# Kernel optimization log

Measured on AMD Instinct MI355X. Metric: run time of the kernel, lower is better.

## Reference

```python
import jax, jax.numpy as jnp
import numpy as np

KSIZE = 7
STRIDE = 4
SCALE = 10.0


def _same_pad(n, k, s):
    # torch 'same' padding used in extract_image_patches (asymmetric)
    out = -(-n // s)
    pad = max(0, (out - 1) * s + k - n)
    top = pad // 2
    return (top, pad - top)


def _conv1x1(x, W, b):
    # x: [C,H,W], W: [O,C], b: [O]
    return jnp.einsum('oc,chw->ohw', W, x) + b[:, None, None]


def _unfold(x, k, s, pad_h, pad_w):
    # x: [C,H,W] -> patches [Lh*Lw, C*k*k] in (C, kh, kw) order (torch Unfold order)
    C = x.shape[0]
    xp = jnp.pad(x, ((0, 0), pad_h, pad_w))
    Hp, Wp = xp.shape[1], xp.shape[2]
    Lh = (Hp - k) // s + 1
    Lw = (Wp - k) // s + 1
    ih = (jnp.arange(Lh) * s)[:, None] + jnp.arange(k)  # [Lh,k]
    iw = (jnp.arange(Lw) * s)[:, None] + jnp.arange(k)  # [Lw,k]
    p = xp[:, ih][:, :, :, iw]                # [C,Lh,k,Lw,k]
    p = p.transpose(1, 3, 0, 2, 4).reshape(Lh * Lw, C * k * k)
    return p, Lh, Lw


def _fold(p, Lh, Lw, C, k, s, H, W, pad):
    # p: [Lh*Lw, C*k*k] -> overlap-summed image [C,H,W] (torch F.fold, symmetric pad)
    P = p.reshape(Lh, Lw, C, k, k).transpose(2, 0, 1, 3, 4)  # [C,Lh,Lw,k,k]
    Hp, Wp = H + 2 * pad, W + 2 * pad
    ih = (jnp.arange(Lh) * s)[:, None] + jnp.arange(k)  # [Lh,k]
    iw = (jnp.arange(Lw) * s)[:, None] + jnp.arange(k)  # [Lw,k]
    IH = ih[:, None, :, None]  # broadcast -> [Lh,Lw,k,k]
    IW = iw[None, :, None, :]
    canvas = jnp.zeros((C, Hp, Wp), p.dtype).at[:, IH, IW].add(P)
    return canvas[:, pad:pad + H, pad:pad + W]


def _salsa_one(x, Wg, bg, Wt, bt, Wp, bp, Ww, bw):
    # x: [C,H,W]
    C, H, W = x.shape
    ic = Wg.shape[0]
    k, s = KSIZE, STRIDE
    ph = _same_pad(H, k, s)
    pw = _same_pad(W, k, s)
    q, Lh, Lw = _unfold(_conv1x1(x, Wg, bg), k, s, ph, pw)   # g   -> queries [L, ic*k*k]
    kk, _, _ = _unfold(_conv1x1(x, Wp, bp), k, s, ph, pw)    # phi -> keys
    v, _, _ = _unfold(_conv1x1(x, Wt, bt), k, s, ph, pw)     # theta -> values
    att = jax.nn.softmax((q @ kk.T) * SCALE, axis=1)         # [L1,L2]
    out = att @ v                                            # [L1, ic*k*k]
    fp = (k - 1) // 2  # paddings[0] from stride-1 same_padding in the original (=3)
    zi = _fold(out, Lh, Lw, ic, k, s, H, W, fp)
    ones_p, mLh, mLw = _unfold(jnp.ones((ic, H, W), x.dtype), k, s, (fp, fp), (fp, fp))
    mask = _fold(ones_p, mLh, mLw, ic, k, s, H, W, fp)
    zi = zi / mask
    return x + _conv1x1(zi, Ww, bw)


def setup_inputs() -> dict:
    key = jax.random.key(0)
    B, C, H, W, IC = 4, 64, 256, 256, 16
    ks = jax.random.split(key, 9)
    sC = 1.0 / np.sqrt(C)
    sI = 1.0 / np.sqrt(IC)
    return {
        'b': jax.random.normal(ks[0], (B, C, H, W), jnp.float32),
        'Wg': jax.random.normal(ks[1], (IC, C), jnp.float32) * sC,
        'bg': jax.random.normal(ks[2], (IC,), jnp.float32) * 0.01,
        'Wt': jax.random.normal(ks[3], (IC, C), jnp.float32) * sC,
        'bt': jax.random.normal(ks[4], (IC,), jnp.float32) * 0.01,
        'Wp': jax.random.normal(ks[5], (IC, C), jnp.float32) * sC,
        'bp': jax.random.normal(ks[6], (IC,), jnp.float32) * 0.01,
        'Ww': jax.random.normal(ks[7], (C, IC), jnp.float32) * sI,
        'bw': jax.random.normal(ks[8], (C,), jnp.float32) * 0.01,
    }


def reference(b, Wg, bg, Wt, bt, Wp, bp, Ww, bw):
    f = jax.vmap(_salsa_one, in_axes=(0, None, None, None, None, None, None, None, None))
    return f(b, Wg, bg, Wt, bt, Wp, bp, Ww, bw)
```

## Files before the change

### kernel.cpp

```cpp
#include <hip/hip_runtime.h>

#define CIN 64
#define ICN 16
#define HH 256
#define WID 256
#define HW (HH*WID)
#define LL 4096
#define KD 784
#define KDP 800
#define KQ 832
#define NVT 896
#define NB 4
#define SPLITK 4
#define KCH (LL/SPLITK)

typedef __attribute__((ext_vector_type(8))) short short8;
typedef __attribute__((ext_vector_type(4))) float f32x4;
typedef __attribute__((ext_vector_type(4))) int i32x4;

__device__ __forceinline__ unsigned short f2bf(float x){
  union { float f; unsigned u; } v; v.f = x;
  unsigned r = v.u + 0x7FFF + ((v.u >> 16) & 1);
  return (unsigned short)(r >> 16);
}

__global__ __launch_bounds__(256) void conv1x1_3(
    const float* __restrict__ x,
    const float* __restrict__ Wg, const float* __restrict__ bg,
    const float* __restrict__ Wp, const float* __restrict__ bp,
    const float* __restrict__ Wt, const float* __restrict__ bt,
    float* __restrict__ G, float* __restrict__ P, float* __restrict__ T) {
  __shared__ float wg[ICN*CIN], wp[ICN*CIN], wt[ICN*CIN];
  int t = threadIdx.x;
  for (int i = t; i < ICN*CIN; i += 256) { wg[i]=Wg[i]; wp[i]=Wp[i]; wt[i]=Wt[i]; }
  __syncthreads();
  int p = blockIdx.x*256 + t;
  float aG[ICN], aP[ICN], aT[ICN];
#pragma unroll
  for (int o=0;o<ICN;o++){ aG[o]=bg[o]; aP[o]=bp[o]; aT[o]=bt[o]; }
  for (int c=0;c<CIN;c++){
    float xv = x[c*HW + p];
#pragma unroll
    for (int o=0;o<ICN;o++){
      aG[o] = fmaf(wg[o*CIN+c], xv, aG[o]);
      aP[o] = fmaf(wp[o*CIN+c], xv, aP[o]);
      aT[o] = fmaf(wt[o*CIN+c], xv, aT[o]);
    }
  }
#pragma unroll
  for (int o=0;o<ICN;o++){ G[o*HW+p]=aG[o]; P[o*HW+p]=aP[o]; T[o*HW+p]=aT[o]; }
}

__global__ __launch_bounds__(256) void unfold_qk_q(
    const float* __restrict__ G, const float* __restrict__ P,
    char* __restrict__ Q0, char* __restrict__ Q1,
    char* __restrict__ K0, char* __restrict__ K1,
    float* __restrict__ sQ, float* __restrict__ sK){
  __shared__ float gb[KQ], pb[KQ];
  __shared__ float redg[256], redp[256];
  int row = blockIdx.x;
  int iy = row >> 6, ix = row & 63;
  int t = threadIdx.x;
  float gmax = 0.f, pmax = 0.f;
  for (int col = t; col < KQ; col += 256){
    float g = 0.f, p = 0.f;
    if (col < KD){
      int c = col / 49; int r = col - c*49; int dy = r / 7; int dx = r - dy*7;
      int y = (iy<<2) + dy - 1, x = (ix<<2) + dx - 1;
      if ((unsigned)y < HH && (unsigned)x < WID){
        int a = c*HW + (y<<8) + x;
        g = G[a]; p = P[a];
      }
    }
    gb[col] = g; pb[col] = p;
    gmax = fmaxf(gmax, fabsf(g)); pmax = fmaxf(pmax, fabsf(p));
  }
  redg[t]=gmax; redp[t]=pmax; __syncthreads();
  for (int s2=128;s2>0;s2>>=1){
    if (t<s2){ redg[t]=fmaxf(redg[t],redg[t+s2]); redp[t]=fmaxf(redp[t],redp[t+s2]); }
    __syncthreads();
  }
  float mg = redg[0], mp = redp[0];
  float rsg = mg > 0.f ? mg*(1.f/127.f) : 1.f;
  float rsp = mp > 0.f ? mp*(1.f/127.f) : 1.f;
  if (t==0){ sQ[row]=rsg; sK[row]=rsp; }
  float ig = 1.f/rsg, ip = 1.f/rsp;
  if (t < KQ/4){
    char q0[4],q1[4],k0[4],k1[4];
#pragma unroll
    for (int u=0;u<4;u++){
      float xg = gb[t*4+u]*ig;
      float a0 = rintf(xg);
      int ia1 = (int)rintf((xg - a0)*256.f);
      ia1 = ia1>127?127:(ia1<-127?-127:ia1);
      q0[u] = (char)(int)a0; q1[u] = (char)ia1;
      float xp = pb[t*4+u]*ip;
      float b0 = rintf(xp);
      int ib1 = (int)rintf((xp - b0)*256.f);
      ib1 = ib1>127?127:(ib1<-127?-127:ib1);
      k0[u] = (char)(int)b0; k1[u] = (char)ib1;
    }
    size_t o = (size_t)row*KQ + t*4;
    *(char4*)(Q0+o) = make_char4(q0[0],q0[1],q0[2],q0[3]);
    *(char4*)(Q1+o) = make_char4(q1[0],q1[1],q1[2],q1[3]);
    *(char4*)(K0+o) = make_char4(k0[0],k0[1],k0[2],k0[3]);
    *(char4*)(K1+o) = make_char4(k1[0],k1[1],k1[2],k1[3]);
  }
}

__global__ __launch_bounds__(256) void unfold_vt(
    const float* __restrict__ T, unsigned short* __restrict__ Vt){
  int idx = blockIdx.x*256 + threadIdx.x;
  int col = idx >> 12, row = idx & 4095;
  float t = 0.f;
  if (col < KD){
    int c = col / 49; int r = col - c*49; int dy = r / 7; int dx = r - dy*7;
    int iy = row >> 6, ix = row & 63;
    int y = (iy<<2) + dy - 1, x = (ix<<2) + dx - 1;
    if ((unsigned)y < HH && (unsigned)x < WID) t = T[c*HW + (y<<8) + x];
  }
  Vt[idx] = f2bf(t);
}

__global__ __launch_bounds__(256) void gemm_qk_i8(
    const char* __restrict__ Q0, const char* __restrict__ Q1,
    const char* __restrict__ K0, const char* __restrict__ K1,
    const float* __restrict__ sQ, const float* __restrict__ sK,
    float* __restrict__ ATT){
  __shared__ alignas(16) char lds[4][128*64];
  const int tid = threadIdx.x;
  const int lane = tid & 63, w = tid >> 6;
  const int wr = w >> 1, wc = w & 1;
  const int row0 = blockIdx.y*128, col0 = blockIdx.x*128;

  const char* base;
  { const char* s0[4] = {
      Q0 + (size_t)row0*KQ, Q1 + (size_t)row0*KQ,
      K0 + (size_t)col0*KQ, K1 + (size_t)col0*KQ };
    base = s0[w]; }

  const int r_lo = lane >> 2, slot = lane & 3;
  int goff[8];
#pragma unroll
  for (int j=0;j<8;j++){
    int r = j*16 + r_lo;
    goff[j] = r*KQ + ((slot ^ ((r>>1)&3))<<4);
  }

  const int lrow = lane & 15, g = lane >> 4;
  int offA[4], offB[4];
#pragma unroll
  for (int i=0;i<4;i++){
    int rA = wr*64 + i*16 + lrow;
    offA[i] = rA*64 + ((g ^ ((rA>>1)&3))<<4);
    int rB = wc*64 + i*16 + lrow;
    offB[i] = rB*64 + ((g ^ ((rB>>1)&3))<<4);
  }

  i32x4 accH[4][4] = {};
  i32x4 accC[4][4] = {};

  for (int kb = 0; kb < KQ; kb += 64){
#pragma unroll
    for (int j=0;j<8;j++)
      __builtin_amdgcn_global_load_lds(
        (const __attribute__((address_space(1))) void*)(base + goff[j] + kb),
        (__attribute__((address_space(3))) void*)(&lds[w][j*1024]), 16, 0, 0);
    __syncthreads();
    i32x4 a0[4], a1[4], b0[4], b1[4];
#pragma unroll
    for (int i=0;i<4;i++){
      a0[i] = *(const i32x4*)&lds[0][offA[i]];
      a1[i] = *(const i32x4*)&lds[1][offA[i]];
      b0[i] = *(const i32x4*)&lds[2][offB[i]];
      b1[i] = *(const i32x4*)&lds[3][offB[i]];
    }
#pragma unroll
    for (int i=0;i<4;i++)
#pragma unroll
      for (int j=0;j<4;j++){
        accH[i][j] = __builtin_amdgcn_mfma_i32_16x16x64_i8(a0[i], b0[j], accH[i][j], 0,0,0);
        accC[i][j] = __builtin_amdgcn_mfma_i32_16x16x64_i8(a0[i], b1[j], accC[i][j], 0,0,0);
        accC[i][j] = __builtin_amdgcn_mfma_i32_16x16x64_i8(a1[i], b0[j], accC[i][j], 0,0,0);
      }
    __syncthreads();
  }

#pragma unroll
  for (int j=0;j<4;j++){
    int col = col0 + wc*64 + j*16 + lrow;
    float cs = sK[col]*10.f;
#pragma unroll
    for (int i=0;i<4;i++){
#pragma unroll
      for (int r=0;r<4;r++){
        int row = row0 + wr*64 + i*16 + g*4 + r;
        float rs = sQ[row];
        ATT[(size_t)row*LL + col] =
          rs*cs*((float)accH[i][j][r] + (float)accC[i][j][r]*0.00390625f);
      }
    }
  }
}

__global__ __launch_bounds__(256) void softmax_rows(
    const float* __restrict__ ATT, unsigned short* __restrict__ Pb){
  __shared__ float red[256];
  int t = threadIdx.x;
  const float4* r4 = (const float4*)(ATT + (size_t)blockIdx.x * LL);
  ushort4* po = (ushort4*)(Pb + (size_t)blockIdx.x * LL);
  float4 v[4];
  float mx = -3.4e38f;
#pragma unroll
  for (int i=0;i<4;i++){
    v[i] = r4[t + (i<<8)];
    mx = fmaxf(mx, fmaxf(fmaxf(v[i].x, v[i].y), fmaxf(v[i].z, v[i].w)));
  }
  red[t] = mx; __syncthreads();
  for (int s2=128;s2>0;s2>>=1){ if (t<s2) red[t]=fmaxf(red[t],red[t+s2]); __syncthreads(); }
  mx = red[0]; __syncthreads();
  float sum = 0.f;
#pragma unroll
  for (int i=0;i<4;i++){
    v[i].x = __expf(v[i].x-mx); v[i].y = __expf(v[i].y-mx);
    v[i].z = __expf(v[i].z-mx); v[i].w = __expf(v[i].w-mx);
    sum += v[i].x + v[i].y + v[i].z + v[i].w;
  }
  red[t]=sum; __syncthreads();
  for (int s2=128;s2>0;s2>>=1){ if (t<s2) red[t]+=red[t+s2]; __syncthreads(); }
  float inv = 1.0f / red[0];
#pragma unroll
  for (int i=0;i<4;i++){
    ushort4 o;
    o.x = f2bf(v[i].x*inv); o.y = f2bf(v[i].y*inv);
    o.z = f2bf(v[i].z*inv); o.w = f2bf(v[i].w*inv);
    po[t + (i<<8)] = o;
  }
}

__global__ __launch_bounds__(256) void gemm_pv_mfma(
    const unsigned short* __restrict__ Pb, const unsigned short* __restrict__ Vt,
    float* __restrict__ OUTP){
  __shared__ alignas(16) short ldsA[128*32];
  __shared__ alignas(16) short ldsB[128*32];
  const int tid = threadIdx.x;
  const int lane = tid & 63, w = tid >> 6;
  const int wr = w >> 1, wc = w & 1;
  const int row0 = blockIdx.y*128, col0 = blockIdx.x*128;
  const int z = blockIdx.z;
  float* OUT = OUTP + (size_t)z * LL * KDP;

  const unsigned short* baseA = Pb + (size_t)row0*LL;
  const unsigned short* baseB = Vt + (size_t)col0*LL;
  const int r_lo = lane >> 2, slot = lane & 3;
  int goff0, goff1;
  { int r = w*16 + r_lo;       goff0 = r*LL + ((slot ^ ((r>>1)&3))<<3); }
  { int r = (4+w)*16 + r_lo;   goff1 = r*LL + ((slot ^ ((r>>1)&3))<<3); }

  const int lrow = lane & 15, g = lane >> 4;
  int offA[4], offB[4];
#pragma unroll
  for (int i=0;i<4;i++){
    int rA = wr*64 + i*16 + lrow;
    offA[i] = rA*32 + ((g ^ ((rA>>1)&3))<<3);
    int rB = wc*64 + i*16 + lrow;
    offB[i] = rB*32 + ((g ^ ((rB>>1)&3))<<3);
  }

  f32x4 acc[4][4] = {};

  const int kend = (z+1)*KCH;
  for (int kb = z*KCH; kb < kend; kb += 32){
    __builtin_amdgcn_global_load_lds(
      (const __attribute__((address_space(1))) void*)(baseA + goff0 + kb),
      (__attribute__((address_space(3))) void*)(&ldsA[w*512]), 16, 0, 0);
    __builtin_amdgcn_global_load_lds(
      (const __attribute__((address_space(1))) void*)(baseA + goff1 + kb),
      (__attribute__((address_space(3))) void*)(&ldsA[(4+w)*512]), 16, 0, 0);
    __builtin_amdgcn_global_load_lds(
      (const __attribute__((address_space(1))) void*)(baseB + goff0 + kb),
      (__attribute__((address_space(3))) void*)(&ldsB[w*512]), 16, 0, 0);
    __builtin_amdgcn_global_load_lds(
      (const __attribute__((address_space(1))) void*)(baseB + goff1 + kb),
      (__attribute__((address_space(3))) void*)(&ldsB[(4+w)*512]), 16, 0, 0);
    __syncthreads();
    short8 a[4], b[4];
#pragma unroll
    for (int i=0;i<4;i++){
      a[i] = *(const short8*)&ldsA[offA[i]];
      b[i] = *(const short8*)&ldsB[offB[i]];
    }
#pragma unroll
    for (int i=0;i<4;i++)
#pragma unroll
      for (int j=0;j<4;j++)
        acc[i][j] = __builtin_amdgcn_mfma_f32_16x16x32_bf16(a[i], b[j], acc[i][j], 0,0,0);
    __syncthreads();
  }

#pragma unroll
  for (int i=0;i<4;i++)
#pragma unroll
    for (int j=0;j<4;j++){
      int col = col0 + wc*64 + j*16 + lrow;
      if (col < KD){
#pragma unroll
        for (int r=0;r<4;r++)
          OUT[(size_t)(row0 + wr*64 + i*16 + g*4 + r)*KDP + col] = acc[i][j][r];
      }
    }
}

__global__ __launch_bounds__(256) void pv_reduce(float* __restrict__ P){
  const size_t PL = (size_t)LL*KDP/4;
  size_t idx = (size_t)blockIdx.x*256 + threadIdx.x;
  if (idx >= PL) return;
  float4* p = (float4*)P;
  float4 a = p[idx], b = p[idx+PL], c = p[idx+2*PL], d = p[idx+3*PL];
  a.x += b.x + c.x + d.x;
  a.y += b.y + c.y + d.y;
  a.z += b.z + c.z + d.z;
  a.w += b.w + c.w + d.w;
  p[idx] = a;
}

__global__ __launch_bounds__(256) void fold_final(
    const float* __restrict__ OUT, const float* __restrict__ xin,
    const float* __restrict__ Ww, const float* __restrict__ bw,
    float* __restrict__ out){
  __shared__ float wsh[CIN*ICN];
  __shared__ float bsh[CIN];
  int t = threadIdx.x;
  for (int i=t;i<CIN*ICN;i+=256) wsh[i]=Ww[i];
  if (t<CIN) bsh[t]=bw[t];
  __syncthreads();
  int p = blockIdx.x*256 + t;
  int y = p >> 8, x = p & 255;
  int yc = y + 3, xc = x + 3;
  int i0 = (yc-3) >> 2; int i1 = yc >> 2; if (i1 > 63) i1 = 63;
  int j0 = (xc-3) >> 2; int j1 = xc >> 2; if (j1 > 63) j1 = 63;
  float zi[ICN] = {};
  for (int i = i0; i <= i1; i++){
    int dy = yc - (i<<2);
    for (int j = j0; j <= j1; j++){
      int dx = xc - (j<<2);
      const float* bp = &OUT[(size_t)((i<<6)+j)*KDP + dy*7 + dx];
#pragma unroll
      for (int c=0;c<ICN;c++) zi[c] += bp[c*49];
    }
  }
  float inv = 1.0f / (float)((i1-i0+1)*(j1-j0+1));
#pragma unroll
  for (int c=0;c<ICN;c++) zi[c] *= inv;
#pragma unroll
  for (int co=0;co<CIN;co++){
    float acc = xin[co*HW + p] + bsh[co];
    const float4* w4 = (const float4*)&wsh[co*ICN];
#pragma unroll
    for (int c4=0;c4<4;c4++){
      float4 wv = w4[c4];
      acc = fmaf(wv.x, zi[c4*4+0], acc);
      acc = fmaf(wv.y, zi[c4*4+1], acc);
      acc = fmaf(wv.z, zi[c4*4+2], acc);
      acc = fmaf(wv.w, zi[c4*4+3], acc);
    }
    out[co*HW + p] = acc;
  }
}

extern "C" void kernel_launch(void* const* d_in, const int* in_sizes, int n_in,
                              void* d_out, int out_size, void* d_ws, size_t ws_size,
                              hipStream_t stream) {
  const float* xb = (const float*)d_in[0];
  const float* Wg = (const float*)d_in[1];
  const float* bg = (const float*)d_in[2];
  const float* Wt = (const float*)d_in[3];
  const float* bt = (const float*)d_in[4];
  const float* Wp = (const float*)d_in[5];
  const float* bp = (const float*)d_in[6];
  const float* Ww = (const float*)d_in[7];
  const float* bw = (const float*)d_in[8];
  float* out = (float*)d_out;

  char* ws = (char*)d_ws;
  float*          G   = (float*)(ws + 0);
  float*          Pc  = (float*)(ws + 4194304);
  float*          T   = (float*)(ws + 8388608);
  char*           Q0  = (char*)(ws + 12582912);
  char*           Q1  = (char*)(ws + 15990784);
  char*           K0  = (char*)(ws + 19398656);
  char*           K1  = (char*)(ws + 22806528);
  float*          sQ  = (float*)(ws + 26214400);
  float*          sK  = (float*)(ws + 26230784);
  float*          ATT = (float*)(ws + 33554432);
  unsigned short* Vt  = (unsigned short*)(ws + 100663296);
  unsigned short* Pb  = (unsigned short*)(ws + 0);
  float*          OUTP= (float*)(ws + 33554432);

  for (int b = 0; b < NB; b++){
    const float* x = xb + (size_t)b*CIN*HW;
    conv1x1_3<<<HW/256, 256, 0, stream>>>(x, Wg,bg, Wp,bp, Wt,bt, G,Pc,T);
    unfold_qk_q<<<LL, 256, 0, stream>>>(G, Pc, Q0, Q1, K0, K1, sQ, sK);
    unfold_vt<<<NVT*LL/256, 256, 0, stream>>>(T, Vt);
    gemm_qk_i8<<<dim3(LL/128, LL/128), 256, 0, stream>>>(Q0, Q1, K0, K1, sQ, sK, ATT);
    softmax_rows<<<LL, 256, 0, stream>>>(ATT, Pb);
    gemm_pv_mfma<<<dim3(NVT/128, LL/128, SPLITK), 256, 0, stream>>>(Pb, Vt, OUTP);
    pv_reduce<<<(LL*KDP/4 + 255)/256, 256, 0, stream>>>(OUTP);
    fold_final<<<HW/256, 256, 0, stream>>>(OUTP, x, Ww, bw, out + (size_t)b*CIN*HW);
  }
}
```

Baseline: 1.191 ms.

## Shrink GEMM tiles to 64x64 with XCD-aware block remapping and wider K step

Both the int8 QK GEMM and the bf16 PV GEMM move from 128x128 to 64x64 output tiles, which raises block count and occupancy. A flat block index is permuted with stride-8 interleaving so that consecutive blocks spread across XCDs. The PV kernel now advances K by 64 per iteration, uses an 8-way XOR swizzle, and gives A loads to two waves and B loads to the other two. Smaller tiles lower per-block data reuse and increase global and L2 traffic, which trades arithmetic intensity for parallelism.

```diff
diff --git a/kernel.cpp b/kernel.cpp
--- a/kernel.cpp
+++ b/kernel.cpp
@@ -127,11 +127,13 @@
     const char* __restrict__ K0, const char* __restrict__ K1,
     const float* __restrict__ sQ, const float* __restrict__ sK,
     float* __restrict__ ATT){
-  __shared__ alignas(16) char lds[4][128*64];
+  __shared__ alignas(16) char lds[4][64*64];
   const int tid = threadIdx.x;
   const int lane = tid & 63, w = tid >> 6;
   const int wr = w >> 1, wc = w & 1;
-  const int row0 = blockIdx.y*128, col0 = blockIdx.x*128;
+  int flat = blockIdx.y * 64 + blockIdx.x;
+  int nf = (flat & 7) * 512 + (flat >> 3);
+  const int row0 = (nf >> 6) * 64, col0 = (nf & 63) * 64;
 
   const char* base;
   { const char* s0[4] = {
@@ -140,45 +142,45 @@
     base = s0[w]; }
 
   const int r_lo = lane >> 2, slot = lane & 3;
-  int goff[8];
-#pragma unroll
-  for (int j=0;j<8;j++){
+  int goff[4];
+#pragma unroll
+  for (int j=0;j<4;j++){
     int r = j*16 + r_lo;
     goff[j] = r*KQ + ((slot ^ ((r>>1)&3))<<4);
   }
 
   const int lrow = lane & 15, g = lane >> 4;
-  int offA[4], offB[4];
-#pragma unroll
-  for (int i=0;i<4;i++){
-    int rA = wr*64 + i*16 + lrow;
+  int offA[2], offB[2];
+#pragma unroll
+  for (int i=0;i<2;i++){
+    int rA = wr*32 + i*16 + lrow;
     offA[i] = rA*64 + ((g ^ ((rA>>1)&3))<<4);
-    int rB = wc*64 + i*16 + lrow;
+    int rB = wc*32 + i*16 + lrow;
     offB[i] = rB*64 + ((g ^ ((rB>>1)&3))<<4);
   }
 
-  i32x4 accH[4][4] = {};
-  i32x4 accC[4][4] = {};
+  i32x4 accH[2][2] = {};
+  i32x4 accC[2][2] = {};
 
   for (int kb = 0; kb < KQ; kb += 64){
 #pragma unroll
-    for (int j=0;j<8;j++)
+    for (int j=0;j<4;j++)
       __builtin_amdgcn_global_load_lds(
         (const __attribute__((address_space(1))) void*)(base + goff[j] + kb),
         (__attribute__((address_space(3))) void*)(&lds[w][j*1024]), 16, 0, 0);
     __syncthreads();
-    i32x4 a0[4], a1[4], b0[4], b1[4];
-#pragma unroll
-    for (int i=0;i<4;i++){
+    i32x4 a0[2], a1[2], b0[2], b1[2];
+#pragma unroll
+    for (int i=0;i<2;i++){
       a0[i] = *(const i32x4*)&lds[0][offA[i]];
       a1[i] = *(const i32x4*)&lds[1][offA[i]];
       b0[i] = *(const i32x4*)&lds[2][offB[i]];
       b1[i] = *(const i32x4*)&lds[3][offB[i]];
     }
 #pragma unroll
-    for (int i=0;i<4;i++)
-#pragma unroll
-      for (int j=0;j<4;j++){
+    for (int i=0;i<2;i++)
+#pragma unroll
+      for (int j=0;j<2;j++){
         accH[i][j] = __builtin_amdgcn_mfma_i32_16x16x64_i8(a0[i], b0[j], accH[i][j], 0,0,0);
         accC[i][j] = __builtin_amdgcn_mfma_i32_16x16x64_i8(a0[i], b1[j], accC[i][j], 0,0,0);
         accC[i][j] = __builtin_amdgcn_mfma_i32_16x16x64_i8(a1[i], b0[j], accC[i][j], 0,0,0);
@@ -187,14 +189,14 @@
   }
 
 #pragma unroll
-  for (int j=0;j<4;j++){
-    int col = col0 + wc*64 + j*16 + lrow;
+  for (int j=0;j<2;j++){
+    int col = col0 + wc*32 + j*16 + lrow;
     float cs = sK[col]*10.f;
 #pragma unroll
-    for (int i=0;i<4;i++){
+    for (int i=0;i<2;i++){
 #pragma unroll
       for (int r=0;r<4;r++){
-        int row = row0 + wr*64 + i*16 + g*4 + r;
+        int row = row0 + wr*32 + i*16 + g*4 + r;
         float rs = sQ[row];
         ATT[(size_t)row*LL + col] =
           rs*cs*((float)accH[i][j][r] + (float)accC[i][j][r]*0.00390625f);
@@ -241,72 +243,87 @@
 __global__ __launch_bounds__(256) void gemm_pv_mfma(
     const unsigned short* __restrict__ Pb, const unsigned short* __restrict__ Vt,
     float* __restrict__ OUTP){
-  __shared__ alignas(16) short ldsA[128*32];
-  __shared__ alignas(16) short ldsB[128*32];
+  __shared__ alignas(16) short ldsA[64*64];
+  __shared__ alignas(16) short ldsB[64*64];
   const int tid = threadIdx.x;
   const int lane = tid & 63, w = tid >> 6;
   const int wr = w >> 1, wc = w & 1;
-  const int row0 = blockIdx.y*128, col0 = blockIdx.x*128;
+  int flat = blockIdx.y * 14 + blockIdx.x;
+  int nf = (flat & 7) * 112 + (flat >> 3);
+  const int col0 = (nf % 14) * 64, row0 = (nf / 14) * 64;
   const int z = blockIdx.z;
   float* OUT = OUTP + (size_t)z * LL * KDP;
 
   const unsigned short* baseA = Pb + (size_t)row0*LL;
   const unsigned short* baseB = Vt + (size_t)col0*LL;
-  const int r_lo = lane >> 2, slot = lane & 3;
-  int goff0, goff1;
-  { int r = w*16 + r_lo;       goff0 = r*LL + ((slot ^ ((r>>1)&3))<<3); }
-  { int r = (4+w)*16 + r_lo;   goff1 = r*LL + ((slot ^ ((r>>1)&3))<<3); }
+
+  const int r8 = lane >> 3, slot8 = lane & 7;
+  int goffs[4];
+  const int jj0 = (w & 1) * 4;
+#pragma unroll
+  for (int j=0;j<4;j++){
+    int r = (jj0 + j)*8 + r8;
+    goffs[j] = r*LL + ((slot8 ^ (r&7))<<3);
+  }
 
   const int lrow = lane & 15, g = lane >> 4;
-  int offA[4], offB[4];
-#pragma unroll
-  for (int i=0;i<4;i++){
-    int rA = wr*64 + i*16 + lrow;
-    offA[i] = rA*32 + ((g ^ ((rA>>1)&3))<<3);
-    int rB = wc*64 + i*16 + lrow;
-    offB[i] = rB*32 + ((g ^ ((rB>>1)&3))<<3);
-  }
-
-  f32x4 acc[4][4] = {};
+  int offA[2][2], offB[2][2];
+#pragma unroll
+  for (int i=0;i<2;i++){
+    int rA = wr*32 + i*16 + lrow;
+    int rB = wc*32 + i*16 + lrow;
+#pragma unroll
+    for (int s=0;s<2;s++){
+      offA[i][s] = rA*64 + (((s*4+g) ^ (rA&7))<<3);
+      offB[i][s] = rB*64 + (((s*4+g) ^ (rB&7))<<3);
+    }
+  }
+
+  f32x4 acc[2][2] = {};
 
   const int kend = (z+1)*KCH;
-  for (int kb = z*KCH; kb < kend; kb += 32){
-    __builtin_amdgcn_global_load_lds(
-      (const __attribute__((address_space(1))) void*)(baseA + goff0 + kb),
-      (__attribute__((address_space(3))) void*)(&ldsA[w*512]), 16, 0, 0);
-    __builtin_amdgcn_global_load_lds(
-      (const __attribute__((address_space(1))) void*)(baseA + goff1 + kb),
-      (__attribute__((address_space(3))) void*)(&ldsA[(4+w)*512]), 16, 0, 0);
-    __builtin_amdgcn_global_load_lds(
-      (const __attribute__((address_space(1))) void*)(baseB + goff0 + kb),
-      (__attribute__((address_space(3))) void*)(&ldsB[w*512]), 16, 0, 0);
-    __builtin_amdgcn_global_load_lds(
-      (const __attribute__((address_space(1))) void*)(baseB + goff1 + kb),
-      (__attribute__((address_space(3))) void*)(&ldsB[(4+w)*512]), 16, 0, 0);
+  for (int kb = z*KCH; kb < kend; kb += 64){
+    if (w < 2){
+#pragma unroll
+      for (int j=0;j<4;j++)
+        __builtin_amdgcn_global_load_lds(
+          (const __attribute__((address_space(1))) void*)(baseA + goffs[j] + kb),
+          (__attribute__((address_space(3))) void*)((char*)ldsA + (jj0+j)*1024), 16, 0, 0);
+    } else {
+#pragma unroll
+      for (int j=0;j<4;j++)
+        __builtin_amdgcn_global_load_lds(
+          (const __attribute__((address_space(1))) void*)(baseB + goffs[j] + kb),
+          (__attribute__((address_space(3))) void*)((char*)ldsB + (jj0+j)*1024), 16, 0, 0);
+    }
     __syncthreads();
-    short8 a[4], b[4];
-#pragma unroll
-    for (int i=0;i<4;i++){
-      a[i] = *(const short8*)&ldsA[offA[i]];
-      b[i] = *(const short8*)&ldsB[offB[i]];
-    }
-#pragma unroll
-    for (int i=0;i<4;i++)
-#pragma unroll
-      for (int j=0;j<4;j++)
-        acc[i][j] = __builtin_amdgcn_mfma_f32_16x16x32_bf16(a[i], b[j], acc[i][j], 0,0,0);
+    short8 a[2][2], b[2][2];
+#pragma unroll
+    for (int i=0;i<2;i++)
+#pragma unroll
+      for (int s=0;s<2;s++){
+        a[i][s] = *(const short8*)&ldsA[offA[i][s]];
+        b[i][s] = *(const short8*)&ldsB[offB[i][s]];
+      }
+#pragma unroll
+    for (int s=0;s<2;s++)
+#pragma unroll
+      for (int i=0;i<2;i++)
+#pragma unroll
+        for (int j=0;j<2;j++)
+          acc[i][j] = __builtin_amdgcn_mfma_f32_16x16x32_bf16(a[i][s], b[j][s], acc[i][j], 0,0,0);
     __syncthreads();
   }
 
 #pragma unroll
-  for (int i=0;i<4;i++)
-#pragma unroll
-    for (int j=0;j<4;j++){
-      int col = col0 + wc*64 + j*16 + lrow;
+  for (int i=0;i<2;i++)
+#pragma unroll
+    for (int j=0;j<2;j++){
+      int col = col0 + wc*32 + j*16 + lrow;
       if (col < KD){
 #pragma unroll
         for (int r=0;r<4;r++)
-          OUT[(size_t)(row0 + wr*64 + i*16 + g*4 + r)*KDP + col] = acc[i][j][r];
+          OUT[(size_t)(row0 + wr*32 + i*16 + g*4 + r)*KDP + col] = acc[i][j][r];
       }
     }
 }
@@ -402,9 +419,9 @@
     conv1x1_3<<<HW/256, 256, 0, stream>>>(x, Wg,bg, Wp,bp, Wt,bt, G,Pc,T);
     unfold_qk_q<<<LL, 256, 0, stream>>>(G, Pc, Q0, Q1, K0, K1, sQ, sK);
     unfold_vt<<<NVT*LL/256, 256, 0, stream>>>(T, Vt);
-    gemm_qk_i8<<<dim3(LL/128, LL/128), 256, 0, stream>>>(Q0, Q1, K0, K1, sQ, sK, ATT);
+    gemm_qk_i8<<<dim3(64, 64), 256, 0, stream>>>(Q0, Q1, K0, K1, sQ, sK, ATT);
     softmax_rows<<<LL, 256, 0, stream>>>(ATT, Pb);
-    gemm_pv_mfma<<<dim3(NVT/128, LL/128, SPLITK), 256, 0, stream>>>(Pb, Vt, OUTP);
+    gemm_pv_mfma<<<dim3(14, 64, SPLITK), 256, 0, stream>>>(Pb, Vt, OUTP);
     pv_reduce<<<(LL*KDP/4 + 255)/256, 256, 0, stream>>>(OUTP);
     fold_final<<<HW/256, 256, 0, stream>>>(OUTP, x, Ww, bw, out + (size_t)b*CIN*HW);
   }
```

Measured after the change: 1.094 ms. 1.09x faster.
